# Kernel tuning notes

Hardware: AMD Instinct MI355X
Metric: run time of the kernel (lower is better)

## Reference

```python
import jax, jax.numpy as jnp
import numpy as np

N = 100000   # nodes
E = 2500000  # edges (before self-loops)
G = 64       # graphs in the batch


def _glorot(key, fi, fo):
    return jax.random.normal(key, (fi, fo), jnp.float32) * jnp.sqrt(2.0 / (fi + fo))


def setup_inputs() -> dict:
    key = jax.random.key(0)
    ks = jax.random.split(key, 8)
    x = jax.random.normal(ks[0], (N, 3), jnp.float32)
    edge_index = jax.random.randint(ks[1], (2, E), 0, N)
    batch = jnp.sort(jax.random.randint(ks[2], (N,), 0, G))
    return dict(
        x=x, edge_index=edge_index, batch=batch,
        W1=_glorot(ks[3], 3, 16),  b1=jnp.zeros((16,), jnp.float32),
        W2=_glorot(ks[4], 16, 32), b2=jnp.zeros((32,), jnp.float32),
        W3=_glorot(ks[5], 32, 16), b3=jnp.zeros((16,), jnp.float32),
        W4=_glorot(ks[6], 16, 2),  b4=jnp.zeros((2,), jnp.float32),
    )


def reference(x, edge_index, batch, W1, b1, W2, b2, W3, b3, W4, b4):
    # PyG GCNConv: add self-loops, sym-normalize by deg^{-1/2}, gather->scatter-add.
    loops = jnp.arange(N)
    src = jnp.concatenate([edge_index[0], loops])  # [E+N]
    dst = jnp.concatenate([edge_index[1], loops])
    deg = jax.ops.segment_sum(jnp.ones_like(dst, jnp.float32), dst, num_segments=N)
    dinv = jax.lax.rsqrt(jnp.maximum(deg, 1.0))  # deg >= 1 due to self-loops
    norm = (dinv[src] * dinv[dst])[:, None]      # [E+N, 1]

    def gcn_conv(h, W, b):
        h = h @ W                                  # [N, out]
        msg = h[src] * norm                        # gather + edge scaling
        agg = jax.ops.segment_sum(msg, dst, num_segments=N)  # scatter-add
        return agg + b

    h = jax.nn.relu(gcn_conv(x, W1, b1))
    h = jax.nn.relu(gcn_conv(h, W2, b2))
    h = jax.nn.relu(gcn_conv(h, W3, b3))
    # F.dropout with training=False (module in eval) is identity
    h = gcn_conv(h, W4, b4)                        # [N, 2]

    # global_mean_pool over graph ids
    sums = jax.ops.segment_sum(h, batch, num_segments=G)
    cnts = jax.ops.segment_sum(jnp.ones((N,), h.dtype), batch, num_segments=G)
    pooled = sums / jnp.maximum(cnts, 1.0)[:, None]  # [G, 2]
    return jax.nn.log_softmax(pooled, axis=1)
```

## Files before the change

### kernel.cpp

```cpp
#include <hip/hip_runtime.h>
#include <hip/hip_fp16.h>
#include <cmath>

static constexpr int NN = 100000;
static constexpr int NE = 2500000;
static constexpr int NG = 64;
static constexpr int BSH = 7;
static constexpr int NBUCK = (NN + 127) / 128;
static constexpr int CSH = 12;
static constexpr int CHUNK = 4096;
static constexpr int NCHUNK = (NE + CHUNK - 1) / CHUNK;

union H4 { float2 f2; __half2 h2[2]; };

__device__ inline void unpack_add_fp8x16(float* a, const int4 r) {
    auto f = __builtin_amdgcn_cvt_pk_f32_fp8(r.x, false); a[0] += f[0];  a[1] += f[1];
    f = __builtin_amdgcn_cvt_pk_f32_fp8(r.x, true);       a[2] += f[0];  a[3] += f[1];
    f = __builtin_amdgcn_cvt_pk_f32_fp8(r.y, false);      a[4] += f[0];  a[5] += f[1];
    f = __builtin_amdgcn_cvt_pk_f32_fp8(r.y, true);       a[6] += f[0];  a[7] += f[1];
    f = __builtin_amdgcn_cvt_pk_f32_fp8(r.z, false);      a[8] += f[0];  a[9] += f[1];
    f = __builtin_amdgcn_cvt_pk_f32_fp8(r.z, true);       a[10] += f[0]; a[11] += f[1];
    f = __builtin_amdgcn_cvt_pk_f32_fp8(r.w, false);      a[12] += f[0]; a[13] += f[1];
    f = __builtin_amdgcn_cvt_pk_f32_fp8(r.w, true);       a[14] += f[0]; a[15] += f[1];
}

__device__ inline void store_fp8_pair(unsigned* row_words, int p, float f0, float f1) {
    unsigned my = ((unsigned)__builtin_amdgcn_cvt_pk_fp8_f32(f0, f1, 0, false)) & 0xFFFFu;
    unsigned nb = (unsigned)__shfl_xor((int)my, 1);
    if ((p & 1) == 0) row_words[p >> 1] = my | (nb << 16);
}

__global__ void p1_hist(const int* __restrict__ dst, int* __restrict__ Ht) {
    __shared__ int hist[NBUCK];
    int t = threadIdx.x, c = blockIdx.x;
    for (int i = t; i < NBUCK; i += 256) hist[i] = 0;
    __syncthreads();
    int e0 = c * CHUNK, e1 = min(e0 + CHUNK, NE);
    for (int e = e0 + t; e < e1; e += 256) atomicAdd(&hist[dst[e] >> BSH], 1);
    __syncthreads();
    for (int b = t; b < NBUCK; b += 256) Ht[(size_t)b * NCHUNK + c] = hist[b];
}

__global__ void p2_scan(int* __restrict__ Ht, int* __restrict__ count,
                        float* __restrict__ pooled3) {
    __shared__ int s[256];
    int b = blockIdx.x, t = threadIdx.x;
    if (b == 0 && t < NG * 3) pooled3[t] = 0.0f;
    int* row = Ht + (size_t)b * NCHUNK;
    int carry = 0;
    for (int seg = 0; seg < 3; ++seg) {
        int idx = seg * 256 + t;
        int v = (idx < NCHUNK) ? row[idx] : 0;
        __syncthreads();
        s[t] = v;
        __syncthreads();
#pragma unroll
        for (int off = 1; off < 256; off <<= 1) {
            int y = (t >= off) ? s[t - off] : 0;
            __syncthreads();
            s[t] += y;
            __syncthreads();
        }
        int incl = s[t];
        int segtot = s[255];
        if (idx < NCHUNK) row[idx] = incl - v + carry;
        carry += segtot;
    }
    if (t == 0) count[b] = carry;
}

__global__ void p3_scatter(const int* __restrict__ src, const int* __restrict__ dst,
                           const int* __restrict__ Ht, int* __restrict__ staging) {
    __shared__ int cur[NBUCK];
    int t = threadIdx.x, bid = blockIdx.x;
    int x = bid & 7, o = bid >> 3;
    int len = 76 + (x < 3 ? 1 : 0);
    if (o >= len) return;
    int c = x * 76 + min(x, 3) + o;
    for (int b = t; b < NBUCK; b += 256) cur[b] = Ht[(size_t)b * NCHUNK + c];
    __syncthreads();
    int e0 = c * CHUNK, e1 = min(e0 + CHUNK, NE);
    for (int e = e0 + t; e < e1; e += 256) {
        int d = dst[e];
        int b = d >> BSH;
        int r = atomicAdd(&cur[b], 1);
        staging[((size_t)b << CSH) + r] = src[e] | ((d & 127) << 17);
    }
}

__global__ void csr_build_kernel(const int* __restrict__ staging, const int* __restrict__ count,
                                 const float* __restrict__ x,
                                 unsigned* __restrict__ rsd, float* __restrict__ dinv,
                                 int* __restrict__ csr_src, float2* __restrict__ xsh) {
    __shared__ int hist[256];
    __shared__ int scn[256];
    __shared__ int cur[256];
    int b = blockIdx.x, t = threadIdx.x;
    int cnt = count[b];
    int base = b << CSH;
    hist[t] = 0;
    __syncthreads();
    const int* st = staging + ((size_t)b << CSH);
    for (int i = t; i < cnt; i += 256) atomicAdd(&hist[st[i] >> 17], 1);
    __syncthreads();
    int h = hist[t];
    scn[t] = h; __syncthreads();
#pragma unroll
    for (int off = 1; off < 256; off <<= 1) {
        int y = (t >= off) ? scn[t - off] : 0;
        __syncthreads();
        scn[t] += y;
        __syncthreads();
    }
    int ex = scn[t] - h;
    int v = (b << BSH) + t;
    if (t < 128 && v < NN) {
        float dv = rsqrtf((float)h + 1.0f);
        rsd[v]  = (unsigned)(base + ex) | ((unsigned)h << 23);
        dinv[v] = dv;
        H4 u;
        u.h2[0] = __floats2half2_rn(x[v * 3] * dv, x[v * 3 + 1] * dv);
        u.h2[1] = __floats2half2_rn(x[v * 3 + 2] * dv, 0.0f);
        xsh[v] = u.f2;
    }
    cur[t] = ex;
    __syncthreads();
    for (int i = t; i < cnt; i += 256) {
        int p = st[i];
        int r = atomicAdd(&cur[p >> 17], 1);
        csr_src[base + r] = p & 0x1FFFF;
    }
}

__global__ void __launch_bounds__(256) agg3t1_kernel(const float2* __restrict__ xsh,
        const int* __restrict__ csr, const unsigned* __restrict__ rsd,
        const float* __restrict__ dinv, const float* __restrict__ W1,
        const float* __restrict__ b1, unsigned* __restrict__ g2b) {
    __shared__ float sW1[48], sb1[16];
    int t = threadIdx.x;
    if (t < 48) sW1[t] = W1[t];
    if (t < 16) sb1[t] = b1[t];
    __syncthreads();
    int tid = blockIdx.x * 256 + t;
    int v = tid >> 3, p = tid & 7;
    if (v >= NN) return;
    float a0 = 0.0f, a1 = 0.0f, a2 = 0.0f;
    if (p == 0) {
        H4 u; u.f2 = xsh[v];
        float2 f0 = __half22float2(u.h2[0]), f1 = __half22float2(u.h2[1]);
        a0 = f0.x; a1 = f0.y; a2 = f1.x;
    }
    unsigned rd = rsd[v];
    int s0 = rd & 0x7FFFFF, cnt = (int)(rd >> 23);
    int j = p;
    for (; j + 8 < cnt; j += 16) {
        int s1 = csr[s0 + j];
        int s2 = csr[s0 + j + 8];
        H4 u1; u1.f2 = xsh[s1];
        H4 u2; u2.f2 = xsh[s2];
        float2 f0 = __half22float2(u1.h2[0]), f1 = __half22float2(u1.h2[1]);
        a0 += f0.x; a1 += f0.y; a2 += f1.x;
        f0 = __half22float2(u2.h2[0]); f1 = __half22float2(u2.h2[1]);
        a0 += f0.x; a1 += f0.y; a2 += f1.x;
    }
    if (j < cnt) {
        H4 u; u.f2 = xsh[csr[s0 + j]];
        float2 f0 = __half22float2(u.h2[0]), f1 = __half22float2(u.h2[1]);
        a0 += f0.x; a1 += f0.y; a2 += f1.x;
    }
    a0 += __shfl_xor(a0, 1); a1 += __shfl_xor(a1, 1); a2 += __shfl_xor(a2, 1);
    a0 += __shfl_xor(a0, 2); a1 += __shfl_xor(a1, 2); a2 += __shfl_xor(a2, 2);
    a0 += __shfl_xor(a0, 4); a1 += __shfl_xor(a1, 4); a2 += __shfl_xor(a2, 4);
    float dv = dinv[v];
    a0 *= dv; a1 *= dv; a2 *= dv;
    float f[2];
#pragma unroll
    for (int k = 0; k < 2; ++k) {
        int fo = p * 2 + k;
        float g = fmaf(a0, sW1[fo], fmaf(a1, sW1[16 + fo], fmaf(a2, sW1[32 + fo], sb1[fo])));
        f[k] = fmaxf(g, 0.0f) * dv;
    }
    store_fp8_pair(g2b + (size_t)v * 4, p, f[0], f[1]);
}

__global__ void __launch_bounds__(256) agg16mid_kernel(const int4* __restrict__ g2b,
        const int* __restrict__ csr, const unsigned* __restrict__ rsd,
        const float* __restrict__ dinv, const float* __restrict__ W2,
        const float* __restrict__ b2, const float* __restrict__ W3,
        unsigned* __restrict__ g3b) {
    __shared__ float sW2[512], sW3t[512], sb2[32];
    int t = threadIdx.x;
    for (int i = t; i < 512; i += 256) {
        sW2[i] = W2[i];
        int fo = i >> 5, fi = i & 31;
        sW3t[i] = W3[fi * 16 + fo];
    }
    if (t < 32) sb2[t] = b2[t];
    __syncthreads();
    int tid = blockIdx.x * 256 + t;
    int v = tid >> 3, p = tid & 7;
    if (v >= NN) return;
    float a[16];
#pragma unroll
    for (int f = 0; f < 16; ++f) a[f] = 0.0f;
    if (p == 0) unpack_add_fp8x16(a, g2b[v]);
    unsigned rd = rsd[v];
    int s0 = rd & 0x7FFFFF, cnt = (int)(rd >> 23);
    int j = p;
    for (; j + 24 < cnt; j += 32) {
        int s1 = csr[s0 + j];
        int s2 = csr[s0 + j + 8];
        int s3 = csr[s0 + j + 16];
        int s4 = csr[s0 + j + 24];
        int4 xa = g2b[s1], xb = g2b[s2], xc = g2b[s3], xd = g2b[s4];
        unpack_add_fp8x16(a, xa); unpack_add_fp8x16(a, xb);
        unpack_add_fp8x16(a, xc); unpack_add_fp8x16(a, xd);
    }
    for (; j + 8 < cnt; j += 16) {
        int s1 = csr[s0 + j];
        int s2 = csr[s0 + j + 8];
        int4 xa = g2b[s1], xb = g2b[s2];
        unpack_add_fp8x16(a, xa); unpack_add_fp8x16(a, xb);
    }
    if (j < cnt) {
        int4 xa = g2b[csr[s0 + j]];
        unpack_add_fp8x16(a, xa);
    }
#pragma unroll
    for (int f = 0; f < 16; ++f) a[f] += __shfl_xor(a[f], 1);
#pragma unroll
    for (int f = 0; f < 16; ++f) a[f] += __shfl_xor(a[f], 2);
#pragma unroll
    for (int f = 0; f < 16; ++f) a[f] += __shfl_xor(a[f], 4);
    float dv = dinv[v];
#pragma unroll
    for (int f = 0; f < 16; ++f) a[f] *= dv;
    float h2p[4];
#pragma unroll
    for (int k = 0; k < 4; ++k) {
        int fo = p * 4 + k;
        float s = sb2[fo];
#pragma unroll
        for (int fi = 0; fi < 16; ++fi) s = fmaf(a[fi], sW2[fi * 32 + fo], s);
        h2p[k] = fmaxf(s, 0.0f);
    }
    float po[16];
#pragma unroll
    for (int fo = 0; fo < 16; ++fo) {
        const float* wrow = sW3t + fo * 32 + p * 4;
        float s = h2p[0] * wrow[0];
        s = fmaf(h2p[1], wrow[1], s);
        s = fmaf(h2p[2], wrow[2], s);
        s = fmaf(h2p[3], wrow[3], s);
        po[fo] = s;
    }
#pragma unroll
    for (int f = 0; f < 16; ++f) po[f] += __shfl_xor(po[f], 1);
#pragma unroll
    for (int f = 0; f < 16; ++f) po[f] += __shfl_xor(po[f], 2);
#pragma unroll
    for (int f = 0; f < 16; ++f) po[f] += __shfl_xor(po[f], 4);
    store_fp8_pair(g3b + (size_t)v * 4, p, po[p * 2] * dv, po[p * 2 + 1] * dv);
}

__global__ void __launch_bounds__(256) agg16t4_kernel(const int4* __restrict__ g3b,
        const int* __restrict__ csr, const unsigned* __restrict__ rsd,
        const float* __restrict__ dinv, const float* __restrict__ b3,
        const float* __restrict__ W4, float2* __restrict__ g4) {
    __shared__ float sb3[16], sW4[32];
    int t = threadIdx.x;
    if (t < 16) sb3[t] = b3[t];
    if (t < 32) sW4[t] = W4[t];
    __syncthreads();
    int tid = blockIdx.x * 256 + t;
    int v = tid >> 3, p = tid & 7;
    if (v >= NN) return;
    float a[16];
#pragma unroll
    for (int f = 0; f < 16; ++f) a[f] = 0.0f;
    if (p == 0) unpack_add_fp8x16(a, g3b[v]);
    unsigned rd = rsd[v];
    int s0 = rd & 0x7FFFFF, cnt = (int)(rd >> 23);
    int j = p;
    for (; j + 24 < cnt; j += 32) {
        int s1 = csr[s0 + j];
        int s2 = csr[s0 + j + 8];
        int s3 = csr[s0 + j + 16];
        int s4 = csr[s0 + j + 24];
        int4 xa = g3b[s1], xb = g3b[s2], xc = g3b[s3], xd = g3b[s4];
        unpack_add_fp8x16(a, xa); unpack_add_fp8x16(a, xb);
        unpack_add_fp8x16(a, xc); unpack_add_fp8x16(a, xd);
    }
    for (; j + 8 < cnt; j += 16) {
        int s1 = csr[s0 + j];
        int s2 = csr[s0 + j + 8];
        int4 xa = g3b[s1], xb = g3b[s2];
        unpack_add_fp8x16(a, xa); unpack_add_fp8x16(a, xb);
    }
    if (j < cnt) {
        int4 xa = g3b[csr[s0 + j]];
        unpack_add_fp8x16(a, xa);
    }
#pragma unroll
    for (int f = 0; f < 16; ++f) a[f] += __shfl_xor(a[f], 1);
#pragma unroll
    for (int f = 0; f < 16; ++f) a[f] += __shfl_xor(a[f], 2);
#pragma unroll
    for (int f = 0; f < 16; ++f) a[f] += __shfl_xor(a[f], 4);
    float dv = dinv[v];
    int f0 = p * 2, f1 = p * 2 + 1;
    float h3a = fmaxf(fmaf(a[f0], dv, sb3[f0]), 0.0f);
    float h3b = fmaxf(fmaf(a[f1], dv, sb3[f1]), 0.0f);
    float o0 = fmaf(h3a, sW4[f0 * 2 + 0], h3b * sW4[f1 * 2 + 0]);
    float o1 = fmaf(h3a, sW4[f0 * 2 + 1], h3b * sW4[f1 * 2 + 1]);
    o0 += __shfl_xor(o0, 1); o1 += __shfl_xor(o1, 1);
    o0 += __shfl_xor(o0, 2); o1 += __shfl_xor(o1, 2);
    o0 += __shfl_xor(o0, 4); o1 += __shfl_xor(o1, 4);
    if (p == 0) g4[v] = make_float2(o0 * dv, o1 * dv);
}

__global__ void __launch_bounds__(256) agg2pool_kernel(const float2* __restrict__ g4,
        const int* __restrict__ csr, const unsigned* __restrict__ rsd,
        const float* __restrict__ dinv, const float* __restrict__ b4,
        const int* __restrict__ batch, float* __restrict__ pooled3) {
    __shared__ float spool[NG * 3];
    int t = threadIdx.x;
    for (int i = t; i < NG * 3; i += 256) spool[i] = 0.0f;
    __syncthreads();
    int tid = blockIdx.x * 256 + t;
    int v = tid >> 3, p = tid & 7;
    if (v < NN) {
        float a0 = 0.0f, a1 = 0.0f;
        if (p == 0) { float2 s = g4[v]; a0 = s.x; a1 = s.y; }
        unsigned rd = rsd[v];
        int s0 = rd & 0x7FFFFF, cnt = (int)(rd >> 23);
        int j = p;
        for (; j + 8 < cnt; j += 16) {
            float2 q1 = g4[csr[s0 + j]];
            float2 q2 = g4[csr[s0 + j + 8]];
            a0 += q1.x + q2.x; a1 += q1.y + q2.y;
        }
        if (j < cnt) {
            float2 q = g4[csr[s0 + j]];
            a0 += q.x; a1 += q.y;
        }
        a0 += __shfl_xor(a0, 1); a1 += __shfl_xor(a1, 1);
        a0 += __shfl_xor(a0, 2); a1 += __shfl_xor(a1, 2);
        a0 += __shfl_xor(a0, 4); a1 += __shfl_xor(a1, 4);
        if (p == 0) {
            float dv = dinv[v];
            float o0 = fmaf(a0, dv, b4[0]);
            float o1 = fmaf(a1, dv, b4[1]);
            int gi = batch[v];
            atomicAdd(&spool[gi * 3 + 0], o0);
            atomicAdd(&spool[gi * 3 + 1], o1);
            atomicAdd(&spool[gi * 3 + 2], 1.0f);
        }
    }
    __syncthreads();
    for (int i = t; i < NG * 3; i += 256)
        if (spool[i] != 0.0f) atomicAdd(&pooled3[i], spool[i]);
}

__global__ void lsm_kernel(const float* __restrict__ pooled3, float* __restrict__ out) {
    int g = threadIdx.x;
    if (g < NG) {
        float c = fmaxf(pooled3[g * 3 + 2], 1.0f);
        float a = pooled3[g * 3 + 0] / c;
        float b = pooled3[g * 3 + 1] / c;
        float m = fmaxf(a, b);
        float lse = m + logf(expf(a - m) + expf(b - m));
        out[g * 2 + 0] = a - lse;
        out[g * 2 + 1] = b - lse;
    }
}

extern "C" void kernel_launch(void* const* d_in, const int* in_sizes, int n_in,
                              void* d_out, int out_size, void* d_ws, size_t ws_size,
                              hipStream_t stream) {
    (void)in_sizes; (void)n_in; (void)out_size; (void)ws_size;

    const float* x   = (const float*)d_in[0];
    const int*   ei  = (const int*)d_in[1];
    const int*   bat = (const int*)d_in[2];
    const float* W1  = (const float*)d_in[3];
    const float* b1  = (const float*)d_in[4];
    const float* W2  = (const float*)d_in[5];
    const float* b2  = (const float*)d_in[6];
    const float* W3  = (const float*)d_in[7];
    const float* b3  = (const float*)d_in[8];
    const float* W4  = (const float*)d_in[9];
    const float* b4  = (const float*)d_in[10];
    float* out = (float*)d_out;

    const int* src = ei;
    const int* dst = ei + NE;

    char* w = (char*)d_ws;
    int*      Ht      = (int*)w;      w += ((size_t)NBUCK * NCHUNK * 4 + 15) & ~15ull;
    int*      count   = (int*)w;      w += ((size_t)NBUCK * 4 + 15) & ~15ull;
    int*      staging = (int*)w;      w += ((size_t)NBUCK << CSH) * 4;
    int*      csr_src = (int*)w;      w += ((size_t)NBUCK << CSH) * 4;
    unsigned* rsd     = (unsigned*)w; w += (size_t)NN * 4;
    float*    dinv    = (float*)w;    w += (size_t)NN * 4;
    float2*   xsh     = (float2*)w;   w += (size_t)NN * 8;
    unsigned* g2b     = (unsigned*)w; w += (size_t)NN * 16;
    unsigned* g3b     = (unsigned*)w; w += (size_t)NN * 16;
    float2*   g4      = (float2*)w;   w += (size_t)NN * 8;
    float*    pooled3 = (float*)w;    w += NG * 3 * 4;

    const int gN8 = (NN * 8 + 255) / 256;

    p1_hist<<<NCHUNK, 256, 0, stream>>>(dst, Ht);
    p2_scan<<<NBUCK, 256, 0, stream>>>(Ht, count, pooled3);
    p3_scatter<<<616, 256, 0, stream>>>(src, dst, Ht, staging);
    csr_build_kernel<<<NBUCK, 256, 0, stream>>>(staging, count, x, rsd, dinv, csr_src, xsh);

    agg3t1_kernel<<<gN8, 256, 0, stream>>>(xsh, csr_src, rsd, dinv, W1, b1, g2b);
    agg16mid_kernel<<<gN8, 256, 0, stream>>>((const int4*)g2b, csr_src, rsd, dinv, W2, b2,
                                             W3, g3b);
    agg16t4_kernel<<<gN8, 256, 0, stream>>>((const int4*)g3b, csr_src, rsd, dinv, b3, W4, g4);
    agg2pool_kernel<<<gN8, 256, 0, stream>>>(g4, csr_src, rsd, dinv, b4, bat, pooled3);

    lsm_kernel<<<1, 64, 0, stream>>>(pooled3, out);
}
```

Before: 142.0 us.

## Halve edge chunk size and use nontemporal loads for feature gathers

```diff
diff --git a/kernel.cpp b/kernel.cpp
--- a/kernel.cpp
+++ b/kernel.cpp
@@ -8,10 +8,25 @@
 static constexpr int BSH = 7;
 static constexpr int NBUCK = (NN + 127) / 128;
 static constexpr int CSH = 12;
-static constexpr int CHUNK = 4096;
+static constexpr int CHUNK = 2048;
 static constexpr int NCHUNK = (NE + CHUNK - 1) / CHUNK;
+static constexpr int NSEG = (NCHUNK + 255) / 256;
+static constexpr int PQ = NCHUNK / 8;
+static constexpr int PR = NCHUNK % 8;
 
 union H4 { float2 f2; __half2 h2[2]; };
+
+typedef int   v4i __attribute__((ext_vector_type(4)));
+typedef float v2f __attribute__((ext_vector_type(2)));
+
+__device__ inline int4 ntload16(const int4* p) {
+    v4i r = __builtin_nontemporal_load((const v4i*)p);
+    return make_int4(r.x, r.y, r.z, r.w);
+}
+__device__ inline float2 ntload8(const float2* p) {
+    v2f r = __builtin_nontemporal_load((const v2f*)p);
+    return make_float2(r.x, r.y);
+}
 
 __device__ inline void unpack_add_fp8x16(float* a, const int4 r) {
     auto f = __builtin_amdgcn_cvt_pk_f32_fp8(r.x, false); a[0] += f[0];  a[1] += f[1];
@@ -48,7 +63,7 @@
     if (b == 0 && t < NG * 3) pooled3[t] = 0.0f;
     int* row = Ht + (size_t)b * NCHUNK;
     int carry = 0;
-    for (int seg = 0; seg < 3; ++seg) {
+    for (int seg = 0; seg < NSEG; ++seg) {
         int idx = seg * 256 + t;
         int v = (idx < NCHUNK) ? row[idx] : 0;
         __syncthreads();
@@ -74,9 +89,9 @@
     __shared__ int cur[NBUCK];
     int t = threadIdx.x, bid = blockIdx.x;
     int x = bid & 7, o = bid >> 3;
-    int len = 76 + (x < 3 ? 1 : 0);
+    int len = PQ + (x < PR ? 1 : 0);
     if (o >= len) return;
-    int c = x * 76 + min(x, 3) + o;
+    int c = x * PQ + min(x, PR) + o;
     for (int b = t; b < NBUCK; b += 256) cur[b] = Ht[(size_t)b * NCHUNK + c];
     __syncthreads();
     int e0 = c * CHUNK, e1 = min(e0 + CHUNK, NE);
@@ -156,15 +171,15 @@
     for (; j + 8 < cnt; j += 16) {
         int s1 = csr[s0 + j];
         int s2 = csr[s0 + j + 8];
-        H4 u1; u1.f2 = xsh[s1];
-        H4 u2; u2.f2 = xsh[s2];
+        H4 u1; u1.f2 = ntload8(xsh + s1);
+        H4 u2; u2.f2 = ntload8(xsh + s2);
         float2 f0 = __half22float2(u1.h2[0]), f1 = __half22float2(u1.h2[1]);
         a0 += f0.x; a1 += f0.y; a2 += f1.x;
         f0 = __half22float2(u2.h2[0]); f1 = __half22float2(u2.h2[1]);
         a0 += f0.x; a1 += f0.y; a2 += f1.x;
     }
     if (j < cnt) {
-        H4 u; u.f2 = xsh[csr[s0 + j]];
+        H4 u; u.f2 = ntload8(xsh + csr[s0 + j]);
         float2 f0 = __half22float2(u.h2[0]), f1 = __half22float2(u.h2[1]);
         a0 += f0.x; a1 += f0.y; a2 += f1.x;
     }
@@ -212,18 +227,19 @@
         int s2 = csr[s0 + j + 8];
         int s3 = csr[s0 + j + 16];
         int s4 = csr[s0 + j + 24];
-        int4 xa = g2b[s1], xb = g2b[s2], xc = g2b[s3], xd = g2b[s4];
+        int4 xa = ntload16(g2b + s1), xb = ntload16(g2b + s2);
+        int4 xc = ntload16(g2b + s3), xd = ntload16(g2b + s4);
         unpack_add_fp8x16(a, xa); unpack_add_fp8x16(a, xb);
         unpack_add_fp8x16(a, xc); unpack_add_fp8x16(a, xd);
     }
     for (; j + 8 < cnt; j += 16) {
         int s1 = csr[s0 + j];
         int s2 = csr[s0 + j + 8];
-        int4 xa = g2b[s1], xb = g2b[s2];
+        int4 xa = ntload16(g2b + s1), xb = ntload16(g2b + s2);
         unpack_add_fp8x16(a, xa); unpack_add_fp8x16(a, xb);
     }
     if (j < cnt) {
-        int4 xa = g2b[csr[s0 + j]];
+        int4 xa = ntload16(g2b + csr[s0 + j]);
         unpack_add_fp8x16(a, xa);
     }
 #pragma unroll
@@ -287,18 +303,19 @@
         int s2 = csr[s0 + j + 8];
         int s3 = csr[s0 + j + 16];
         int s4 = csr[s0 + j + 24];
-        int4 xa = g3b[s1], xb = g3b[s2], xc = g3b[s3], xd = g3b[s4];
+        int4 xa = ntload16(g3b + s1), xb = ntload16(g3b + s2);
+        int4 xc = ntload16(g3b + s3), xd = ntload16(g3b + s4);
         unpack_add_fp8x16(a, xa); unpack_add_fp8x16(a, xb);
         unpack_add_fp8x16(a, xc); unpack_add_fp8x16(a, xd);
     }
     for (; j + 8 < cnt; j += 16) {
         int s1 = csr[s0 + j];
         int s2 = csr[s0 + j + 8];
-        int4 xa = g3b[s1], xb = g3b[s2];
+        int4 xa = ntload16(g3b + s1), xb = ntload16(g3b + s2);
         unpack_add_fp8x16(a, xa); unpack_add_fp8x16(a, xb);
     }
     if (j < cnt) {
-        int4 xa = g3b[csr[s0 + j]];
+        int4 xa = ntload16(g3b + csr[s0 + j]);
         unpack_add_fp8x16(a, xa);
     }
 #pragma unroll
@@ -336,12 +353,12 @@
         int s0 = rd & 0x7FFFFF, cnt = (int)(rd >> 23);
         int j = p;
         for (; j + 8 < cnt; j += 16) {
-            float2 q1 = g4[csr[s0 + j]];
-            float2 q2 = g4[csr[s0 + j + 8]];
+            float2 q1 = ntload8(g4 + csr[s0 + j]);
+            float2 q2 = ntload8(g4 + csr[s0 + j + 8]);
             a0 += q1.x + q2.x; a1 += q1.y + q2.y;
         }
         if (j < cnt) {
-            float2 q = g4[csr[s0 + j]];
+            float2 q = ntload8(g4 + csr[s0 + j]);
             a0 += q.x; a1 += q.y;
         }
         a0 += __shfl_xor(a0, 1); a1 += __shfl_xor(a1, 1);
@@ -410,10 +427,11 @@
     float*    pooled3 = (float*)w;    w += NG * 3 * 4;
 
     const int gN8 = (NN * 8 + 255) / 256;
+    const int gP3 = 8 * (PQ + 1);
 
     p1_hist<<<NCHUNK, 256, 0, stream>>>(dst, Ht);
     p2_scan<<<NBUCK, 256, 0, stream>>>(Ht, count, pooled3);
-    p3_scatter<<<616, 256, 0, stream>>>(src, dst, Ht, staging);
+    p3_scatter<<<gP3, 256, 0, stream>>>(src, dst, Ht, staging);
     csr_build_kernel<<<NBUCK, 256, 0, stream>>>(staging, count, x, rsd, dinv, csr_src, xsh);
 
     agg3t1_kernel<<<gN8, 256, 0, stream>>>(xsh, csr_src, rsd, dinv, W1, b1, g2b);
```

Result: slower. 193.5 us (+36.2%).
